# Kernel tuning notes

Hardware: AMD Instinct MI355X
Metric: run time of the kernel (lower is better)

## Reference

```python
import jax, jax.numpy as jnp
import numpy as np

D_MODEL = 1024
NUM_HEADS = 16


def setup_inputs() -> dict:
    key = jax.random.key(0)
    ks = jax.random.split(key, 5)
    B, S, D = 4, 2048, D_MODEL
    # std=1.0 trunc_normal in original init; plain normal is fine for a numeric reference,
    # but scale down to keep logits numerically sane under fp32.
    x = jax.random.normal(ks[0], (B, S, D), dtype=jnp.float32)
    wq = jax.random.normal(ks[1], (D, D), dtype=jnp.float32) * 0.02
    wk = jax.random.normal(ks[2], (D, D), dtype=jnp.float32) * 0.02
    wv = jax.random.normal(ks[3], (D, D), dtype=jnp.float32) * 0.02
    wo = jax.random.normal(ks[4], (D, D), dtype=jnp.float32) * 0.02
    return {"x": x, "q_proj_weight": wq, "k_proj_weight": wk,
            "v_proj_weight": wv, "o_proj_weight": wo}


def reference(x, q_proj_weight, k_proj_weight, v_proj_weight, o_proj_weight):
    B, S, D = x.shape
    H = NUM_HEADS
    dh = D // H
    # unfused QKV projections (weights applied as x @ W.T, matching torch)
    q = jnp.einsum('bsd,ed->bse', x, q_proj_weight).reshape(B, S, H, dh).transpose(0, 2, 1, 3)
    k = jnp.einsum('bsd,ed->bse', x, k_proj_weight).reshape(B, S, H, dh).transpose(0, 2, 1, 3)
    v = jnp.einsum('bsd,ed->bse', x, v_proj_weight).reshape(B, S, H, dh).transpose(0, 2, 1, 3)
    scale = 1.0 / jnp.sqrt(jnp.asarray(dh, dtype=x.dtype))
    scores = jnp.einsum('bhqd,bhkd->bhqk', q, k) * scale  # [B,H,S,S]
    causal = jnp.tril(jnp.ones((S, S), dtype=bool))       # True = keep
    scores = jnp.where(causal[None, None], scores, -jnp.inf)
    attn = jax.nn.softmax(scores, axis=-1)
    out = jnp.einsum('bhqk,bhkd->bhqd', attn, v)           # [B,H,S,dh]
    out = out.transpose(0, 2, 1, 3).reshape(B, S, D)
    return jnp.einsum('bsd,ed->bse', out, o_proj_weight)
```

## Files before the change

### kernel.cpp

```cpp
#include <hip/hip_runtime.h>
#include <hip/hip_bf16.h>
#include <stdint.h>


#define S_LEN 2048
#define DM 1024
#define NH 16
#define NB 4
#define DH 64
#define BS (NB * S_LEN)

#if __has_builtin(__builtin_amdgcn_exp2f)
#define EXP2(x) __builtin_amdgcn_exp2f(x)
#else
#define EXP2(x) __expf((x) * 0.6931471805599453f)
#endif

typedef __attribute__((ext_vector_type(4))) float f32x4;
typedef __attribute__((ext_vector_type(16))) float f32x16;
typedef __attribute__((ext_vector_type(8))) short bf16x8;
typedef __attribute__((ext_vector_type(4))) short s16x4;

static __device__ __forceinline__ float bf2f(short u) {
    union { float f; uint32_t i; } c; c.i = ((uint32_t)(uint16_t)u) << 16; return c.f;
}
static __device__ __forceinline__ short f2bf(float f) {
    union { float f; uint32_t i; } c; c.f = f;
    uint32_t r = (c.i + 0x7FFFu + ((c.i >> 16) & 1u)) >> 16;
    return (short)r;
}

__global__ void cast_kernel(const float* __restrict__ in, short* __restrict__ out, int n4) {
    int i = blockIdx.x * blockDim.x + threadIdx.x;
    if (i >= n4) return;
    f32x4 v = *(const f32x4*)(in + (size_t)i * 4);
    s16x4 o;
    o[0] = f2bf(v[0]); o[1] = f2bf(v[1]); o[2] = f2bf(v[2]); o[3] = f2bf(v[3]);
    *(s16x4*)(out + (size_t)i * 4) = o;
}

__global__ void cast4_kernel(const float* __restrict__ a, const float* __restrict__ b,
                             const float* __restrict__ c, const float* __restrict__ d,
                             short* __restrict__ out, int n4per) {
    int z = blockIdx.y;
    const float* in = z == 0 ? a : z == 1 ? b : z == 2 ? c : d;
    int i = blockIdx.x * blockDim.x + threadIdx.x;
    if (i >= n4per) return;
    f32x4 v = *(const f32x4*)(in + (size_t)i * 4);
    s16x4 o;
    o[0] = f2bf(v[0]); o[1] = f2bf(v[1]); o[2] = f2bf(v[2]); o[3] = f2bf(v[3]);
    *(s16x4*)(out + (size_t)z * n4per * 4 + (size_t)i * 4) = o;
}

template <int MODE>
__global__ __launch_bounds__(256) void gemm_bt(const short* __restrict__ A,
                                               const short* __restrict__ Bm,
                                               void* __restrict__ Cout,
                                               int M, int N, int Kd) {
    __shared__ __align__(16) short lA[2][128 * 32];
    __shared__ __align__(16) short lB[2][128 * 32];
    const int tid = threadIdx.x;
    const int lane = tid & 63;
    const int wave = tid >> 6;
    const int mb = blockIdx.x;
    const int nb = blockIdx.y;
    const int wm = (wave >> 1) * 64;
    const int wn = (wave & 1) * 64;
    const int c16 = lane & 15;
    const int g = lane >> 4;

    auto stage = [&](int buf, int kb) {
        for (int i = 0; i < 2; i++) {
            int row = i * 64 + wave * 16 + (lane >> 2);
            int col = (lane & 3) * 8;
            const short* srcA = A + (size_t)(mb * 128 + row) * Kd + kb * 32 + col;
            const short* srcB = Bm + (size_t)(nb * 128 + row) * Kd + kb * 32 + col;
            __builtin_amdgcn_global_load_lds(
                (const __attribute__((address_space(1))) void*)srcA,
                (__attribute__((address_space(3))) void*)(&lA[buf][i * 2048 + wave * 512]),
                16, 0, 0);
            __builtin_amdgcn_global_load_lds(
                (const __attribute__((address_space(1))) void*)srcB,
                (__attribute__((address_space(3))) void*)(&lB[buf][i * 2048 + wave * 512]),
                16, 0, 0);
        }
    };

    f32x4 acc[4][4];
    f32x4 zero = {0.f, 0.f, 0.f, 0.f};
    for (int i = 0; i < 4; i++)
        for (int j = 0; j < 4; j++) acc[i][j] = zero;

    const int nk = Kd >> 5;
    stage(0, 0);
    __syncthreads();
    for (int t = 0; t < nk; t++) {
        int cur = t & 1;
        if (t + 1 < nk) stage(cur ^ 1, t + 1);
        bf16x8 af[4], bfr[4];
        for (int i = 0; i < 4; i++) {
            af[i]  = *(const bf16x8*)&lA[cur][(wm + i * 16 + c16) * 32 + g * 8];
            bfr[i] = *(const bf16x8*)&lB[cur][(wn + i * 16 + c16) * 32 + g * 8];
        }
        for (int mi = 0; mi < 4; mi++)
            for (int ni = 0; ni < 4; ni++)
                acc[mi][ni] = __builtin_amdgcn_mfma_f32_16x16x32_bf16(af[mi], bfr[ni], acc[mi][ni], 0, 0, 0);
        __syncthreads();
    }

    for (int mi = 0; mi < 4; mi++) {
        int row0 = mb * 128 + wm + mi * 16 + g * 4;
        for (int ni = 0; ni < 4; ni++) {
            int col = nb * 128 + wn + ni * 16 + c16;
            f32x4 a = acc[mi][ni];
            for (int r = 0; r < 4; r++) {
                int rr = row0 + r;
                if (MODE == 0) {
                    ((float*)Cout)[(size_t)rr * N + col] = a[r];
                } else if (MODE == 1) {
                    ((short*)Cout)[(size_t)rr * N + col] = f2bf(a[r]);
                } else {
                    int b = rr >> 11, s = rr & 2047, h = col >> 6, d = col & 63;
                    int kl = s & 31;
                    int pos = kl ^ ((((kl >> 2) ^ (kl >> 3)) & 1) ? 12 : 0);
                    ((short*)Cout)[(((size_t)(b * NH + h) * 64 + (s >> 5)) * 64 + d) * 32 + pos] = f2bf(a[r]);
                }
            }
        }
    }
}

__global__ __launch_bounds__(256, 4) void attn_stg_kernel(const short* __restrict__ Q,
                                                          const short* __restrict__ K,
                                                          const short* __restrict__ Vt,
                                                          short* __restrict__ Oo) {
    __shared__ __align__(16) char stg[4][4608];
    const int lane = threadIdx.x & 63;
    const int wave = threadIdx.x >> 6;
    const int j = blockIdx.x >> 6;
    const int bh = blockIdx.x & 63;
    const int b = bh >> 4, h = bh & 15;
    const int l31 = lane & 31;
    const int hi = lane >> 5;
    const bool three = (j <= 20);

    auto lLp = [&](int w) { return (float*)(stg[w] + 4352); };

    const int qtA = 63 - j, qtB = j;
    const int nkA = qtA + 1, nkB = qtB + 1;
    int qt, t0, t1;
    if (three) {
        if (wave < 3) { qt = qtA; t0 = (nkA * wave) / 3; t1 = (nkA * (wave + 1)) / 3; }
        else          { qt = qtB; t0 = 0; t1 = nkB; }
    } else {
        int half = wave & 1;
        if (wave < 2) { int hh = (nkA + 1) >> 1; qt = qtA; t0 = half ? hh : 0; t1 = half ? nkA : hh; }
        else          { int hh = (nkB + 1) >> 1; qt = qtB; t0 = half ? hh : 0; t1 = half ? nkB : hh; }
    }
    const int q0 = qt * 32;
    const int qrow = q0 + l31;

    const short* Qb = Q + (size_t)b * S_LEN * DM + h * DH;
    const short* Kb = K + (size_t)b * S_LEN * DM + h * DH;
    const short* Vb = Vt + (size_t)bh * S_LEN * DH;
    const float QSCALE = 0.125f * 1.4426950408889634f;

    char* wbK = stg[wave];

    bf16x8 qf[4];
    #pragma unroll
    for (int c = 0; c < 4; c++) {
        bf16x8 t = *(const bf16x8*)(Qb + (size_t)qrow * DM + c * 16 + hi * 8);
        #pragma unroll
        for (int jj = 0; jj < 8; jj++) t[jj] = f2bf(bf2f(t[jj]) * QSCALE);
        qf[c] = t;
    }

    f32x16 o0, o1;
    #pragma unroll
    for (int r = 0; r < 16; r++) { o0[r] = 0.f; o1[r] = 0.f; }
    float l_r = 0.f;

    const int i_ = lane;
    const int kcol = (((i_ & 7) ^ (i_ >> 3)) << 3);
    const int krow = (i_ >> 3);
    const short* ksp = Kb + (size_t)(t0 * 32 + krow) * DM + kcol;
    auto stageK = [&]() {
        #pragma unroll
        for (int c = 0; c < 4; c++)
            __builtin_amdgcn_global_load_lds(
                (const __attribute__((address_space(1))) void*)(ksp + (size_t)c * 8 * DM),
                (__attribute__((address_space(3))) void*)(wbK + c * 1024), 16, 0, 0);
        ksp += 32 * DM;
    };

    const short* vsp = Vb + (size_t)t0 * 2048 + (size_t)l31 * 32 + hi * 8;
    bf16x8 kf[4], vf[4];
    auto loadV = [&]() {
        vf[0] = *(const bf16x8*)(vsp);
        vf[1] = *(const bf16x8*)(vsp + 16);
        vf[2] = *(const bf16x8*)(vsp + 1024);
        vf[3] = *(const bf16x8*)(vsp + 1040);
        vsp += 2048;
    };

    const int kx = (l31 & 7) << 4;
    auto readK = [&]() {
        #pragma unroll
        for (int cc = 0; cc < 4; cc++)
            kf[cc] = *(const bf16x8*)(wbK + l31 * 128 + ((cc * 32 + hi * 16) ^ kx));
    };

    if (t0 < t1) {
        stageK();
        loadV();
        asm volatile("s_waitcnt vmcnt(4)" ::: "memory");
        __builtin_amdgcn_sched_barrier(0);
        readK();
    }

    for (int kb = t0; kb < t1; kb++) {
        const int kbase = kb * 32;
        f32x16 st;
        #pragma unroll
        for (int r = 0; r < 16; r++) st[r] = 0.f;
        __builtin_amdgcn_s_setprio(1);
        st = __builtin_amdgcn_mfma_f32_32x32x16_bf16(kf[0], qf[0], st, 0, 0, 0);
        st = __builtin_amdgcn_mfma_f32_32x32x16_bf16(kf[1], qf[1], st, 0, 0, 0);
        st = __builtin_amdgcn_mfma_f32_32x32x16_bf16(kf[2], qf[2], st, 0, 0, 0);
        st = __builtin_amdgcn_mfma_f32_32x32x16_bf16(kf[3], qf[3], st, 0, 0, 0);
        __builtin_amdgcn_s_setprio(0);

        if (kb + 1 < t1) {
            asm volatile("s_waitcnt lgkmcnt(0)" ::: "memory");
            __builtin_amdgcn_sched_barrier(0);
            stageK();
        }

        float p[16];
        if (kb == qt) {
            #pragma unroll
            for (int r = 0; r < 16; r++) {
                int kl = (r & 3) + 8 * (r >> 2) + 4 * hi;
                float v = (kbase + kl > qrow) ? -1e30f : st[r];
                p[r] = EXP2(v);
            }
        } else {
            #pragma unroll
            for (int r = 0; r < 16; r++) p[r] = EXP2(st[r]);
        }

        float s01 = (p[0] + p[1]) + (p[2] + p[3]);
        float s23 = (p[4] + p[5]) + (p[6] + p[7]);
        float s45 = (p[8] + p[9]) + (p[10] + p[11]);
        float s67 = (p[12] + p[13]) + (p[14] + p[15]);
        l_r += (s01 + s23) + (s45 + s67);

        union { uint32_t u[4]; bf16x8 v; } c0, c1;
        #pragma unroll
        for (int i = 0; i < 4; i++) {
            union { float f; uint32_t u; } a0, a1, b0, b1;
            a0.f = p[2 * i];     a1.f = p[2 * i + 1];
            b0.f = p[8 + 2 * i]; b1.f = p[8 + 2 * i + 1];
            c0.u[i] = __builtin_amdgcn_perm(a1.u, a0.u, 0x07060302u);
            c1.u[i] = __builtin_amdgcn_perm(b1.u, b0.u, 0x07060302u);
        }

        __builtin_amdgcn_s_setprio(1);
        o0 = __builtin_amdgcn_mfma_f32_32x32x16_bf16(vf[0], c0.v, o0, 0, 0, 0);
        o0 = __builtin_amdgcn_mfma_f32_32x32x16_bf16(vf[1], c1.v, o0, 0, 0, 0);
        o1 = __builtin_amdgcn_mfma_f32_32x32x16_bf16(vf[2], c0.v, o1, 0, 0, 0);
        o1 = __builtin_amdgcn_mfma_f32_32x32x16_bf16(vf[3], c1.v, o1, 0, 0, 0);
        __builtin_amdgcn_s_setprio(0);

        if (kb + 1 < t1) {
            loadV();
            asm volatile("s_waitcnt vmcnt(4)" ::: "memory");
            __builtin_amdgcn_sched_barrier(0);
            readK();
        }
    }

    l_r += __shfl_xor(l_r, 32);

    const bool publisher = three ? (wave == 1 || wave == 2) : (wave == 1 || wave == 3);
    if (publisher) {
        short* pb = (short*)stg[wave];
        #pragma unroll
        for (int dc = 0; dc < 2; dc++)
            #pragma unroll
            for (int g2 = 0; g2 < 4; g2++) {
                int d = dc * 32 + g2 * 8 + hi * 4;
                s16x4 v4;
                #pragma unroll
                for (int rr = 0; rr < 4; rr++) v4[rr] = f2bf((dc ? o1 : o0)[g2 * 4 + rr]);
                *(s16x4*)(pb + l31 * 68 + d) = v4;
            }
        if (!hi) lLp(wave)[l31] = l_r;
    }
    if (three && wave == 3) {
        float inv = 1.0f / l_r;
        size_t base = ((size_t)b * S_LEN + qrow) * DM + h * DH;
        #pragma unroll
        for (int dc = 0; dc < 2; dc++)
            #pragma unroll
            for (int g2 = 0; g2 < 4; g2++) {
                s16x4 ov;
                #pragma unroll
                for (int rr = 0; rr < 4; rr++)
                    ov[rr] = f2bf((dc ? o1 : o0)[g2 * 4 + rr] * inv);
                *(s16x4*)(Oo + base + dc * 32 + g2 * 8 + hi * 4) = ov;
            }
    }
    __syncthreads();

    const bool merger = three ? (wave == 0) : (wave == 0 || wave == 2);
    if (merger) {
        const short* p1 = (const short*)stg[wave + 1];
        float L = l_r + lLp(wave + 1)[l31];
        const short* p2 = nullptr;
        if (three) { p2 = (const short*)stg[2]; L += lLp(2)[l31]; }
        float inv = 1.0f / L;
        size_t base = ((size_t)b * S_LEN + qrow) * DM + h * DH;
        #pragma unroll
        for (int dc = 0; dc < 2; dc++)
            #pragma unroll
            for (int g2 = 0; g2 < 4; g2++) {
                int d = dc * 32 + g2 * 8 + hi * 4;
                s16x4 a = *(const s16x4*)(p1 + l31 * 68 + d);
                s16x4 ov;
                #pragma unroll
                for (int rr = 0; rr < 4; rr++) {
                    float acc = (dc ? o1 : o0)[g2 * 4 + rr] + bf2f(a[rr]);
                    if (three) acc += bf2f(p2[l31 * 68 + d + rr]);
                    ov[rr] = f2bf(acc * inv);
                }
                *(s16x4*)(Oo + base + d) = ov;
            }
    }
}

extern "C" void kernel_launch(void* const* d_in, const int* in_sizes, int n_in,
                              void* d_out, int out_size, void* d_ws, size_t ws_size,
                              hipStream_t stream) {
    const float* x  = (const float*)d_in[0];
    const float* wq = (const float*)d_in[1];
    const float* wk = (const float*)d_in[2];
    const float* wv = (const float*)d_in[3];
    const float* wo = (const float*)d_in[4];
    float* out = (float*)d_out;

    short* ws = (short*)d_ws;
    size_t off = 0;
    short* xb  = ws + off; off += (size_t)BS * DM;
    short* wqb = ws + off; off += (size_t)DM * DM;
    short* wkb = ws + off; off += (size_t)DM * DM;
    short* wvb = ws + off; off += (size_t)DM * DM;
    short* wob = ws + off; off += (size_t)DM * DM;
    short* Qb  = ws + off; off += (size_t)BS * DM;
    short* Kb  = ws + off; off += (size_t)BS * DM;
    short* Vtb = ws + off; off += (size_t)BS * DM;
    short* attn_o = xb;

    {
        int n4 = (BS * DM) / 4;
        cast_kernel<<<n4 / 256, 256, 0, stream>>>(x, xb, n4);
        int w4 = (DM * DM) / 4;
        cast4_kernel<<<dim3(w4 / 256, 4), 256, 0, stream>>>(wq, wk, wv, wo, wqb, w4);
    }

    dim3 pgrid(BS / 128, DM / 128);
    gemm_bt<1><<<pgrid, 256, 0, stream>>>(xb, wqb, Qb,  BS, DM, DM);
    gemm_bt<1><<<pgrid, 256, 0, stream>>>(xb, wkb, Kb,  BS, DM, DM);
    gemm_bt<2><<<pgrid, 256, 0, stream>>>(xb, wvb, Vtb, BS, DM, DM);

    attn_stg_kernel<<<dim3(2048), 256, 0, stream>>>(Qb, Kb, Vtb, attn_o);

    gemm_bt<0><<<pgrid, 256, 0, stream>>>(attn_o, wob, out, BS, DM, DM);
}
```

Measured before the change: 194.1 us.

## Split each query tile's KV range across four waves, one tile per block

Replaces the paired-tile scheme, where each block handled a long and a short causal query tile with a mixed wave split, with one query tile per block. The tile's KV range is split evenly across all four waves, and wave 0 merges the three partial outputs from LDS. The grid doubles to 4096 blocks, and work per block now varies strongly with the tile index. This simplifies the control flow and the merge, at the cost of losing the built-in load balancing from pairing tiles and doing more split/merge overhead on short tiles.

```diff
diff --git a/kernel.cpp b/kernel.cpp
--- a/kernel.cpp
+++ b/kernel.cpp
@@ -137,26 +137,17 @@
     __shared__ __align__(16) char stg[4][4608];
     const int lane = threadIdx.x & 63;
     const int wave = threadIdx.x >> 6;
-    const int j = blockIdx.x >> 6;
+    const int qt = 63 - (blockIdx.x >> 6);
     const int bh = blockIdx.x & 63;
     const int b = bh >> 4, h = bh & 15;
     const int l31 = lane & 31;
     const int hi = lane >> 5;
-    const bool three = (j <= 20);
 
     auto lLp = [&](int w) { return (float*)(stg[w] + 4352); };
 
-    const int qtA = 63 - j, qtB = j;
-    const int nkA = qtA + 1, nkB = qtB + 1;
-    int qt, t0, t1;
-    if (three) {
-        if (wave < 3) { qt = qtA; t0 = (nkA * wave) / 3; t1 = (nkA * (wave + 1)) / 3; }
-        else          { qt = qtB; t0 = 0; t1 = nkB; }
-    } else {
-        int half = wave & 1;
-        if (wave < 2) { int hh = (nkA + 1) >> 1; qt = qtA; t0 = half ? hh : 0; t1 = half ? nkA : hh; }
-        else          { int hh = (nkB + 1) >> 1; qt = qtB; t0 = half ? hh : 0; t1 = half ? nkB : hh; }
-    }
+    const int nk = qt + 1;
+    const int t0 = (nk * wave) >> 2;
+    const int t1 = (nk * (wave + 1)) >> 2;
     const int q0 = qt * 32;
     const int qrow = q0 + l31;
 
@@ -283,8 +274,7 @@
 
     l_r += __shfl_xor(l_r, 32);
 
-    const bool publisher = three ? (wave == 1 || wave == 2) : (wave == 1 || wave == 3);
-    if (publisher) {
+    if (wave >= 1) {
         short* pb = (short*)stg[wave];
         #pragma unroll
         for (int dc = 0; dc < 2; dc++)
@@ -298,28 +288,13 @@
             }
         if (!hi) lLp(wave)[l31] = l_r;
     }
-    if (three && wave == 3) {
-        float inv = 1.0f / l_r;
-        size_t base = ((size_t)b * S_LEN + qrow) * DM + h * DH;
-        #pragma unroll
-        for (int dc = 0; dc < 2; dc++)
-            #pragma unroll
-            for (int g2 = 0; g2 < 4; g2++) {
-                s16x4 ov;
-                #pragma unroll
-                for (int rr = 0; rr < 4; rr++)
-                    ov[rr] = f2bf((dc ? o1 : o0)[g2 * 4 + rr] * inv);
-                *(s16x4*)(Oo + base + dc * 32 + g2 * 8 + hi * 4) = ov;
-            }
-    }
     __syncthreads();
 
-    const bool merger = three ? (wave == 0) : (wave == 0 || wave == 2);
-    if (merger) {
-        const short* p1 = (const short*)stg[wave + 1];
-        float L = l_r + lLp(wave + 1)[l31];
-        const short* p2 = nullptr;
-        if (three) { p2 = (const short*)stg[2]; L += lLp(2)[l31]; }
+    if (wave == 0) {
+        const short* p1 = (const short*)stg[1];
+        const short* p2 = (const short*)stg[2];
+        const short* p3 = (const short*)stg[3];
+        float L = l_r + lLp(1)[l31] + lLp(2)[l31] + lLp(3)[l31];
         float inv = 1.0f / L;
         size_t base = ((size_t)b * S_LEN + qrow) * DM + h * DH;
         #pragma unroll
@@ -327,12 +302,14 @@
             #pragma unroll
             for (int g2 = 0; g2 < 4; g2++) {
                 int d = dc * 32 + g2 * 8 + hi * 4;
-                s16x4 a = *(const s16x4*)(p1 + l31 * 68 + d);
+                s16x4 a1 = *(const s16x4*)(p1 + l31 * 68 + d);
+                s16x4 a2 = *(const s16x4*)(p2 + l31 * 68 + d);
+                s16x4 a3 = *(const s16x4*)(p3 + l31 * 68 + d);
                 s16x4 ov;
                 #pragma unroll
                 for (int rr = 0; rr < 4; rr++) {
-                    float acc = (dc ? o1 : o0)[g2 * 4 + rr] + bf2f(a[rr]);
-                    if (three) acc += bf2f(p2[l31 * 68 + d + rr]);
+                    float acc = (dc ? o1 : o0)[g2 * 4 + rr]
+                              + bf2f(a1[rr]) + bf2f(a2[rr]) + bf2f(a3[rr]);
                     ov[rr] = f2bf(acc * inv);
                 }
                 *(s16x4*)(Oo + base + d) = ov;
@@ -374,7 +351,7 @@
     gemm_bt<1><<<pgrid, 256, 0, stream>>>(xb, wkb, Kb,  BS, DM, DM);
     gemm_bt<2><<<pgrid, 256, 0, stream>>>(xb, wvb, Vtb, BS, DM, DM);
 
-    attn_stg_kernel<<<dim3(2048), 256, 0, stream>>>(Qb, Kb, Vtb, attn_o);
+    attn_stg_kernel<<<dim3(4096), 256, 0, stream>>>(Qb, Kb, Vtb, attn_o);
 
     gemm_bt<0><<<pgrid, 256, 0, stream>>>(attn_o, wob, out, BS, DM, DM);
 }
```

After: 196.7 us. No clear change (+1.4%).
